# Kernel tuning notes

Measured on AMD Instinct MI355X. Metric: run time of the kernel, lower is better.

Reference implementation:

```python
import jax, jax.numpy as jnp
import numpy as np

B, S, HID = 2, 2048, 4096
NH, NKV, HD = 32, 8, 128
GRP = NH // NKV          # query heads per kv head
G = 128                  # weight quant group size
FP8_MAX = 448.0          # e4m3 max
EPS = 1e-6


def _rmsnorm(x, w):
    return x * jax.lax.rsqrt(jnp.mean(x * x, axis=-1, keepdims=True) + EPS) * w


def _act_quant(x):
    # per-token fp8 quantization: scale = amax/448, values clipped to fp8 range
    s = jnp.max(jnp.abs(x), axis=-1, keepdims=True) / FP8_MAX
    s = jnp.maximum(s, 1e-6)
    return jnp.clip(x / s, -FP8_MAX, FP8_MAX), s


def _deq_weight(wi4, wscale):
    # wi4: [out, in] int values in [0,16) -> signed int4 [-8,7]
    # wscale: [out, in//G] per-group scales, broadcast along input dim
    return (wi4.astype(jnp.float32) - 8.0) * jnp.repeat(wscale, G, axis=1)


def _rotate_half(x):
    x1, x2 = jnp.split(x, 2, axis=-1)
    return jnp.concatenate([-x2, x1], axis=-1)


def setup_inputs() -> dict:
    key = jax.random.key(0)
    ks = jax.random.split(key, 8)
    hidden_states = jax.random.normal(ks[0], (B, S, HID), dtype=jnp.float32)
    ln_weight = jnp.ones((HID,), dtype=jnp.float32)
    # real RoPE tables
    inv_freq = 1.0 / (10000.0 ** (np.arange(0, HD, 2, dtype=np.float32) / HD))
    ang = np.arange(S, dtype=np.float32)[:, None] * inv_freq[None, :]
    emb = np.concatenate([ang, ang], axis=-1)  # [S, HD]
    cos = jnp.broadcast_to(jnp.asarray(np.cos(emb)), (B, S, HD)).astype(jnp.float32)
    sin = jnp.broadcast_to(jnp.asarray(np.sin(emb)), (B, S, HD)).astype(jnp.float32)
    def wq(k, out, inp):
        ki, ksc = jax.random.split(k)
        wi = jax.random.randint(ki, (out, inp), 0, 16, dtype=jnp.int32)
        sc = jax.random.uniform(ksc, (out, inp // G), dtype=jnp.float32) * 0.01 + 0.001
        return wi, sc
    wq_i4, wq_scale = wq(ks[1], NH * HD, HID)
    wk_i4, wk_scale = wq(ks[2], NKV * HD, HID)
    wv_i4, wv_scale = wq(ks[3], NKV * HD, HID)
    wo_i4, wo_scale = wq(ks[4], HID, NH * HD)
    return dict(hidden_states=hidden_states, ln_weight=ln_weight, cos=cos, sin=sin,
                wq_scale=wq_scale, wk_scale=wk_scale, wv_scale=wv_scale, wo_scale=wo_scale,
                wq_i4=wq_i4, wk_i4=wk_i4, wv_i4=wv_i4, wo_i4=wo_i4)


def reference(hidden_states, ln_weight, cos, sin,
              wq_scale, wk_scale, wv_scale, wo_scale,
              wq_i4, wk_i4, wv_i4, wo_i4):
    b, s, _ = hidden_states.shape
    residual = hidden_states
    h = _rmsnorm(hidden_states, ln_weight)
    qx, qx_s = _act_quant(h)                     # [b,s,HID], [b,s,1]
    q = (qx @ _deq_weight(wq_i4, wq_scale).T) * qx_s
    k = (qx @ _deq_weight(wk_i4, wk_scale).T) * qx_s
    v = (qx @ _deq_weight(wv_i4, wv_scale).T) * qx_s
    q = q.reshape(b, s, NH, HD)
    k = k.reshape(b, s, NKV, HD)
    v = v.reshape(b, s, NKV, HD)
    cse, sne = cos[:, :, None, :], sin[:, :, None, :]
    q = q * cse + _rotate_half(q) * sne
    k = k * cse + _rotate_half(k) * sne
    # GQA causal attention (fp8 fmha numerics emulated in fp32)
    qg = q.reshape(b, s, NKV, GRP, HD)
    scaling = HD ** -0.5
    scores = jnp.einsum('bskgd,btkd->bkgst', qg, k) * scaling  # [b,kv,g,s,t]
    causal = jnp.tril(jnp.ones((s, s), dtype=bool))
    scores = jnp.where(causal, scores, jnp.float32(-1e30))
    p = jax.nn.softmax(scores, axis=-1)
    o = jnp.einsum('bkgst,btkd->bskgd', p, v).reshape(b, s, NH * HD)
    qo, qo_s = _act_quant(o)
    out = (qo @ _deq_weight(wo_i4, wo_scale).T) * qo_s + residual
    return out
```

## Files before the change

### kernel.cpp

```cpp
#include <hip/hip_runtime.h>
#include <stdint.h>

#define HID    4096
#define SLEN   2048
#define BATCH  2
#define NHEADS 32
#define NKVH   8
#define HDIM   128
#define NTOK   (BATCH*SLEN)
#define NQK    (NHEADS*HDIM)
#define NKVD   (NKVH*HDIM)
#define NQKV   (NQK + 2*NKVD)
#define ASTR   (NQK + NKVD)

typedef unsigned short u16;
typedef short short8 __attribute__((ext_vector_type(8)));
typedef float f32x4 __attribute__((ext_vector_type(4)));
typedef int int4v __attribute__((ext_vector_type(4)));
typedef u16 u16x4 __attribute__((ext_vector_type(4)));

static __device__ __forceinline__ u16 f2bf(float f) {
  unsigned u = __builtin_bit_cast(unsigned, f);
  u += 0x7FFFu + ((u >> 16) & 1u);
  return (u16)(u >> 16);
}
static __device__ __forceinline__ float bf2f(u16 h) {
  return __builtin_bit_cast(float, (unsigned)h << 16);
}
static __device__ __forceinline__ void gload_lds16(const void* g, void* l) {
  __builtin_amdgcn_global_load_lds((const __attribute__((address_space(1))) void*)g,
                                   (__attribute__((address_space(3))) void*)l, 16, 0, 0);
}

__global__ __launch_bounds__(256) void k_rmsnorm(const float* __restrict__ x,
                                                 const float* __restrict__ w,
                                                 u16* __restrict__ h) {
  const int row = blockIdx.x;
  const float4* xr = (const float4*)(x + (size_t)row * HID);
  float4 vals[4];
  float ss = 0.f;
#pragma unroll
  for (int i = 0; i < 4; ++i) {
    float4 v = xr[threadIdx.x + i * 256];
    vals[i] = v;
    ss += v.x*v.x + v.y*v.y + v.z*v.z + v.w*v.w;
  }
#pragma unroll
  for (int off = 32; off; off >>= 1) ss += __shfl_xor(ss, off);
  __shared__ float red[4];
  if ((threadIdx.x & 63) == 0) red[threadIdx.x >> 6] = ss;
  __syncthreads();
  ss = red[0] + red[1] + red[2] + red[3];
  const float scale = rsqrtf(ss * (1.f / HID) + 1e-6f);
  u16* hr = h + (size_t)row * HID;
#pragma unroll
  for (int i = 0; i < 4; ++i) {
    int c = (threadIdx.x + i * 256) * 4;
    float4 v = vals[i];
    unsigned lo = (unsigned)f2bf(v.x * scale * w[c])   | ((unsigned)f2bf(v.y * scale * w[c+1]) << 16);
    unsigned hi = (unsigned)f2bf(v.z * scale * w[c+2]) | ((unsigned)f2bf(v.w * scale * w[c+3]) << 16);
    *(unsigned long long*)(hr + c) = ((unsigned long long)hi << 32) | lo;
  }
}

__global__ __launch_bounds__(256) void k_deq(const int* __restrict__ W,
                                             const float* __restrict__ Ws,
                                             u16* __restrict__ out) {
  const int idx = blockIdx.x * 256 + threadIdx.x;
  const int n = idx >> 9;
  const int k8 = (idx & 511) * 8;
  const float sc = Ws[n * 32 + (k8 >> 7)];
  int4v a = *(const int4v*)(W + (size_t)n * HID + k8);
  int4v b = *(const int4v*)(W + (size_t)n * HID + k8 + 4);
  u16 r[8];
#pragma unroll
  for (int j = 0; j < 4; ++j) r[j]     = f2bf((float)(a[j] - 8) * sc);
#pragma unroll
  for (int j = 0; j < 4; ++j) r[j + 4] = f2bf((float)(b[j] - 8) * sc);
  *(short8*)(out + (size_t)n * HID + k8) = *(short8*)r;
}

#define BM 128
#define BN 128
#define BK 64

__global__ __launch_bounds__(256) void k_gemm_qkv_b(
    const u16* __restrict__ A, const u16* __restrict__ B,
    u16* __restrict__ C, u16* __restrict__ Vt) {
  __shared__ __align__(16) u16 lA[BM * BK];
  __shared__ __align__(16) u16 lB[BN * BK];
  const int tid = threadIdx.x;
  const int lane = tid & 63;
  const int wave = tid >> 6;
  const int wm = wave >> 1, wn = wave & 1;
  const int m0 = blockIdx.x * BM;
  const int n0 = blockIdx.y * BN;

  const int rloc = wave * 8 + (lane >> 3);
  const int lb8 = (((lane & 7) ^ (lane >> 3)) << 3);

  f32x4 acc[4][4];
#pragma unroll
  for (int mi = 0; mi < 4; ++mi)
#pragma unroll
    for (int ni = 0; ni < 4; ++ni) acc[mi][ni] = (f32x4){0.f, 0.f, 0.f, 0.f};

  for (int k0 = 0; k0 < HID; k0 += BK) {
    __syncthreads();
#pragma unroll
    for (int p = 0; p < 4; ++p)
      gload_lds16(A + (size_t)(m0 + p * 32 + rloc) * HID + k0 + lb8,
                  lA + p * 2048 + wave * 512);
#pragma unroll
    for (int p = 0; p < 4; ++p)
      gload_lds16(B + (size_t)(n0 + p * 32 + rloc) * HID + k0 + lb8,
                  lB + p * 2048 + wave * 512);
    __syncthreads();
#pragma unroll
    for (int kc = 0; kc < 2; ++kc) {
      const int kOff = kc * 32 + ((lane >> 4) << 3);
      short8 af[4], bfr[4];
#pragma unroll
      for (int i = 0; i < 4; ++i) {
        const int m = wm * 64 + i * 16 + (lane & 15);
        af[i] = *(const short8*)(lA + ((m * 64 + kOff) ^ ((m & 7) << 3)));
        const int n = wn * 64 + i * 16 + (lane & 15);
        bfr[i] = *(const short8*)(lB + ((n * 64 + kOff) ^ ((n & 7) << 3)));
      }
#pragma unroll
      for (int mi = 0; mi < 4; ++mi)
#pragma unroll
        for (int ni = 0; ni < 4; ++ni)
          acc[mi][ni] = __builtin_amdgcn_mfma_f32_16x16x32_bf16(af[mi], bfr[ni], acc[mi][ni], 0, 0, 0);
    }
  }
  if (n0 < ASTR) {
#pragma unroll
    for (int mi = 0; mi < 4; ++mi) {
      const int row = m0 + wm * 64 + mi * 16 + ((lane >> 4) << 2);
#pragma unroll
      for (int ni = 0; ni < 4; ++ni) {
        const int col = n0 + wn * 64 + ni * 16 + (lane & 15);
#pragma unroll
        for (int r = 0; r < 4; ++r)
          C[(size_t)(row + r) * ASTR + col] = f2bf(acc[mi][ni][r]);
      }
    }
  } else {
#pragma unroll
    for (int mi = 0; mi < 4; ++mi) {
      const int row = m0 + wm * 64 + mi * 16 + ((lane >> 4) << 2);
      const int b_ = row >> 11, s_ = row & 2047;
#pragma unroll
      for (int ni = 0; ni < 4; ++ni) {
        const int colv = (n0 - ASTR) + wn * 64 + ni * 16 + (lane & 15);
        u16x4 pk;
#pragma unroll
        for (int r = 0; r < 4; ++r) pk[r] = f2bf(acc[mi][ni][r]);
        *(u16x4*)(Vt + ((size_t)(b_ * NKVH + (colv >> 7)) * HDIM + (colv & 127)) * SLEN + s_) = pk;
      }
    }
  }
}

__global__ __launch_bounds__(256) void k_gemm_o_b(
    const u16* __restrict__ A, const u16* __restrict__ B,
    const float* __restrict__ resid, float* __restrict__ out) {
  __shared__ __align__(16) u16 lA[BM * BK];
  __shared__ __align__(16) u16 lB[BN * BK];
  const int tid = threadIdx.x;
  const int lane = tid & 63;
  const int wave = tid >> 6;
  const int wm = wave >> 1, wn = wave & 1;
  const int m0 = blockIdx.x * BM;
  const int n0 = blockIdx.y * BN;

  const int rloc = wave * 8 + (lane >> 3);
  const int lb8 = (((lane & 7) ^ (lane >> 3)) << 3);

  f32x4 acc[4][4];
#pragma unroll
  for (int mi = 0; mi < 4; ++mi)
#pragma unroll
    for (int ni = 0; ni < 4; ++ni) acc[mi][ni] = (f32x4){0.f, 0.f, 0.f, 0.f};

  for (int k0 = 0; k0 < NQK; k0 += BK) {
    __syncthreads();
#pragma unroll
    for (int p = 0; p < 4; ++p)
      gload_lds16(A + (size_t)(m0 + p * 32 + rloc) * NQK + k0 + lb8,
                  lA + p * 2048 + wave * 512);
#pragma unroll
    for (int p = 0; p < 4; ++p)
      gload_lds16(B + (size_t)(n0 + p * 32 + rloc) * NQK + k0 + lb8,
                  lB + p * 2048 + wave * 512);
    __syncthreads();
#pragma unroll
    for (int kc = 0; kc < 2; ++kc) {
      const int kOff = kc * 32 + ((lane >> 4) << 3);
      short8 af[4], bfr[4];
#pragma unroll
      for (int i = 0; i < 4; ++i) {
        const int m = wm * 64 + i * 16 + (lane & 15);
        af[i] = *(const short8*)(lA + ((m * 64 + kOff) ^ ((m & 7) << 3)));
        const int n = wn * 64 + i * 16 + (lane & 15);
        bfr[i] = *(const short8*)(lB + ((n * 64 + kOff) ^ ((n & 7) << 3)));
      }
#pragma unroll
      for (int mi = 0; mi < 4; ++mi)
#pragma unroll
        for (int ni = 0; ni < 4; ++ni)
          acc[mi][ni] = __builtin_amdgcn_mfma_f32_16x16x32_bf16(af[mi], bfr[ni], acc[mi][ni], 0, 0, 0);
    }
  }
#pragma unroll
  for (int mi = 0; mi < 4; ++mi) {
    const int row = m0 + wm * 64 + mi * 16 + ((lane >> 4) << 2);
#pragma unroll
    for (int ni = 0; ni < 4; ++ni) {
      const int col = n0 + wn * 64 + ni * 16 + (lane & 15);
#pragma unroll
      for (int r = 0; r < 4; ++r) {
        const size_t idx = (size_t)(row + r) * HID + col;
        out[idx] = acc[mi][ni][r] + resid[idx];
      }
    }
  }
}

__global__ __launch_bounds__(256) void k_gemm_qkv(
    const u16* __restrict__ A,
    const int* __restrict__ Wq, const int* __restrict__ Wk, const int* __restrict__ Wv,
    const float* __restrict__ Sq, const float* __restrict__ Sk, const float* __restrict__ Sv,
    u16* __restrict__ C, u16* __restrict__ Vt) {
  __shared__ __align__(16) u16 lA[BM * BK];
  __shared__ __align__(16) u16 lB[BN * BK];
  const int tid = threadIdx.x;
  const int lane = tid & 63;
  const int wave = tid >> 6;
  const int wm = wave >> 1, wn = wave & 1;
  const int m0 = blockIdx.x * BM;
  const int n0 = blockIdx.y * BN;

  const int* W; const float* Ws; int nb;
  if (n0 < NQK)       { W = Wq; Ws = Sq; nb = n0; }
  else if (n0 < ASTR) { W = Wk; Ws = Sk; nb = n0 - NQK; }
  else                { W = Wv; Ws = Sv; nb = n0 - ASTR; }

  const int mloc = wave * 8 + (lane >> 3);
  const int lb8 = (((lane & 7) ^ (lane >> 3)) << 3);

  f32x4 acc[4][4];
#pragma unroll
  for (int mi = 0; mi < 4; ++mi)
#pragma unroll
    for (int ni = 0; ni < 4; ++ni) acc[mi][ni] = (f32x4){0.f, 0.f, 0.f, 0.f};

  for (int k0 = 0; k0 < HID; k0 += BK) {
    __syncthreads();
#pragma unroll
    for (int p = 0; p < 4; ++p)
      gload_lds16(A + (size_t)(m0 + p * 32 + mloc) * HID + k0 + lb8,
                  lA + p * 2048 + wave * 512);
    const int grp = k0 >> 7;
#pragma unroll
    for (int p = 0; p < 8; ++p) {
      const int n = p * 16 + (tid >> 4);
      const int kk = (tid & 15) * 4;
      int4v wv4 = *(const int4v*)(W + (size_t)(nb + n) * HID + k0 + kk);
      const float sc = Ws[(nb + n) * 32 + grp];
      unsigned lo = (unsigned)f2bf((float)(wv4[0] - 8) * sc) |
                    ((unsigned)f2bf((float)(wv4[1] - 8) * sc) << 16);
      unsigned hi = (unsigned)f2bf((float)(wv4[2] - 8) * sc) |
                    ((unsigned)f2bf((float)(wv4[3] - 8) * sc) << 16);
      const int di = (n * 64 + kk) ^ ((n & 7) << 3);
      unsigned* dst = (unsigned*)(lB + di);
      dst[0] = lo; dst[1] = hi;
    }
    __syncthreads();
#pragma unroll
    for (int kc = 0; kc < 2; ++kc) {
      const int kOff = kc * 32 + ((lane >> 4) << 3);
      short8 af[4], bfr[4];
#pragma unroll
      for (int i = 0; i < 4; ++i) {
        const int m = wm * 64 + i * 16 + (lane & 15);
        af[i] = *(const short8*)(lA + ((m * 64 + kOff) ^ ((m & 7) << 3)));
        const int n = wn * 64 + i * 16 + (lane & 15);
        bfr[i] = *(const short8*)(lB + ((n * 64 + kOff) ^ ((n & 7) << 3)));
      }
#pragma unroll
      for (int mi = 0; mi < 4; ++mi)
#pragma unroll
        for (int ni = 0; ni < 4; ++ni)
          acc[mi][ni] = __builtin_amdgcn_mfma_f32_16x16x32_bf16(af[mi], bfr[ni], acc[mi][ni], 0, 0, 0);
    }
  }
  if (n0 < ASTR) {
#pragma unroll
    for (int mi = 0; mi < 4; ++mi) {
      const int row = m0 + wm * 64 + mi * 16 + ((lane >> 4) << 2);
#pragma unroll
      for (int ni = 0; ni < 4; ++ni) {
        const int col = n0 + wn * 64 + ni * 16 + (lane & 15);
#pragma unroll
        for (int r = 0; r < 4; ++r)
          C[(size_t)(row + r) * ASTR + col] = f2bf(acc[mi][ni][r]);
      }
    }
  } else {
#pragma unroll
    for (int mi = 0; mi < 4; ++mi) {
      const int row = m0 + wm * 64 + mi * 16 + ((lane >> 4) << 2);
      const int b_ = row >> 11, s_ = row & 2047;
#pragma unroll
      for (int ni = 0; ni < 4; ++ni) {
        const int colv = (n0 - ASTR) + wn * 64 + ni * 16 + (lane & 15);
        u16x4 pk;
#pragma unroll
        for (int r = 0; r < 4; ++r) pk[r] = f2bf(acc[mi][ni][r]);
        *(u16x4*)(Vt + ((size_t)(b_ * NKVH + (colv >> 7)) * HDIM + (colv & 127)) * SLEN + s_) = pk;
      }
    }
  }
}

__global__ __launch_bounds__(256) void k_gemm_o(
    const u16* __restrict__ A, const int* __restrict__ W, const float* __restrict__ Ws,
    const float* __restrict__ resid, float* __restrict__ out) {
  __shared__ __align__(16) u16 lA[BM * BK];
  __shared__ __align__(16) u16 lB[BN * BK];
  const int tid = threadIdx.x;
  const int lane = tid & 63;
  const int wave = tid >> 6;
  const int wm = wave >> 1, wn = wave & 1;
  const int m0 = blockIdx.x * BM;
  const int n0 = blockIdx.y * BN;

  const int mloc = wave * 8 + (lane >> 3);
  const int lb8 = (((lane & 7) ^ (lane >> 3)) << 3);

  f32x4 acc[4][4];
#pragma unroll
  for (int mi = 0; mi < 4; ++mi)
#pragma unroll
    for (int ni = 0; ni < 4; ++ni) acc[mi][ni] = (f32x4){0.f, 0.f, 0.f, 0.f};

  for (int k0 = 0; k0 < NQK; k0 += BK) {
    __syncthreads();
#pragma unroll
    for (int p = 0; p < 4; ++p)
      gload_lds16(A + (size_t)(m0 + p * 32 + mloc) * NQK + k0 + lb8,
                  lA + p * 2048 + wave * 512);
    const int grp = k0 >> 7;
#pragma unroll
    for (int p = 0; p < 8; ++p) {
      const int n = p * 16 + (tid >> 4);
      const int kk = (tid & 15) * 4;
      int4v wv4 = *(const int4v*)(W + (size_t)(n0 + n) * NQK + k0 + kk);
      const float sc = Ws[(n0 + n) * 32 + grp];
      unsigned lo = (unsigned)f2bf((float)(wv4[0] - 8) * sc) |
                    ((unsigned)f2bf((float)(wv4[1] - 8) * sc) << 16);
      unsigned hi = (unsigned)f2bf((float)(wv4[2] - 8) * sc) |
                    ((unsigned)f2bf((float)(wv4[3] - 8) * sc) << 16);
      const int di = (n * 64 + kk) ^ ((n & 7) << 3);
      unsigned* dst = (unsigned*)(lB + di);
      dst[0] = lo; dst[1] = hi;
    }
    __syncthreads();
#pragma unroll
    for (int kc = 0; kc < 2; ++kc) {
      const int kOff = kc * 32 + ((lane >> 4) << 3);
      short8 af[4], bfr[4];
#pragma unroll
      for (int i = 0; i < 4; ++i) {
        const int m = wm * 64 + i * 16 + (lane & 15);
        af[i] = *(const short8*)(lA + ((m * 64 + kOff) ^ ((m & 7) << 3)));
        const int n = wn * 64 + i * 16 + (lane & 15);
        bfr[i] = *(const short8*)(lB + ((n * 64 + kOff) ^ ((n & 7) << 3)));
      }
#pragma unroll
      for (int mi = 0; mi < 4; ++mi)
#pragma unroll
        for (int ni = 0; ni < 4; ++ni)
          acc[mi][ni] = __builtin_amdgcn_mfma_f32_16x16x32_bf16(af[mi], bfr[ni], acc[mi][ni], 0, 0, 0);
      }
  }
#pragma unroll
  for (int mi = 0; mi < 4; ++mi) {
    const int row = m0 + wm * 64 + mi * 16 + ((lane >> 4) << 2);
#pragma unroll
    for (int ni = 0; ni < 4; ++ni) {
      const int col = n0 + wn * 64 + ni * 16 + (lane & 15);
#pragma unroll
      for (int r = 0; r < 4; ++r) {
        const size_t idx = (size_t)(row + r) * HID + col;
        out[idx] = acc[mi][ni][r] + resid[idx];
      }
    }
  }
}

__global__ __launch_bounds__(256) void k_rope(u16* __restrict__ qk,
                                              const float* __restrict__ cosb,
                                              const float* __restrict__ sinb) {
  const int idx = blockIdx.x * 256 + threadIdx.x;
  const int d = idx & 63;
  const int hh = (idx >> 6) % 40;
  const int t = idx / (64 * 40);
  const int col = (hh < 32) ? hh * HDIM : NQK + (hh - 32) * HDIM;
  u16* p = qk + (size_t)t * ASTR + col;
  const float c = cosb[t * HDIM + d], s = sinb[t * HDIM + d];
  const float x1 = bf2f(p[d]), x2 = bf2f(p[d + 64]);
  p[d]      = f2bf(x1 * c - x2 * s);
  p[d + 64] = f2bf(x2 * c + x1 * s);
}

__global__ __launch_bounds__(256) void k_attn(const u16* __restrict__ qk,
                                              const u16* __restrict__ vt,
                                              u16* __restrict__ o) {
  const int slot = blockIdx.x;
  const int w = (slot & 7) * 128 + (slot >> 3);
  const int qi = 15 - (w & 15);
  const int h = (w >> 4) & 31;
  const int b = w >> 9;
  const int kvh = h >> 2;
  const int q0 = qi * 128;
  const int lane = threadIdx.x & 63, wave = threadIdx.x >> 6;
  const int m = lane & 15, kg = lane >> 4;

  const u16* Qb = qk + (size_t)b * SLEN * ASTR + h * HDIM;
  const u16* Kb = qk + (size_t)b * SLEN * ASTR + NQK + kvh * HDIM;
  const u16* Vb = vt + (size_t)(b * NKVH + kvh) * HDIM * SLEN;

  __shared__ __align__(16) u16 Kt[64 * 128];
  __shared__ __align__(16) u16 Vts[128 * 64];
  __shared__ __align__(16) u16 Pl[4][32 * 72];

  const int qr = q0 + wave * 32;
  short8 qf[2][4];
#pragma unroll
  for (int mi = 0; mi < 2; ++mi)
#pragma unroll
    for (int kc = 0; kc < 4; ++kc)
      qf[mi][kc] = *(const short8*)(Qb + (size_t)(qr + mi * 16 + m) * ASTR + kc * 32 + kg * 8);

  f32x4 oacc[2][8];
#pragma unroll
  for (int mi = 0; mi < 2; ++mi)
#pragma unroll
    for (int n = 0; n < 8; ++n) oacc[mi][n] = (f32x4){0.f, 0.f, 0.f, 0.f};
  float rm[2][4], rl[2][4];
#pragma unroll
  for (int mi = 0; mi < 2; ++mi)
#pragma unroll
    for (int r = 0; r < 4; ++r) { rm[mi][r] = -3.0e38f; rl[mi][r] = 0.f; }

  const float sscale = 0.08838834764831845f;
  const int nt = q0 / 64 + 2;
  for (int t = 0; t < nt; ++t) {
    const int kv0 = t * 64;
    __syncthreads();
#pragma unroll
    for (int p = 0; p < 4; ++p) {
      const int row = p * 16 + wave * 4 + (lane >> 4);
      const int c8s = (lane & 15) ^ (row & 7);
      gload_lds16(Kb + (size_t)(kv0 + row) * ASTR + c8s * 8, Kt + p * 2048 + wave * 512);
    }
#pragma unroll
    for (int p = 0; p < 4; ++p) {
      const int d = p * 32 + wave * 8 + (lane >> 3);
      const int c8s = (lane & 7) ^ (d & 7);
      gload_lds16(Vb + (size_t)d * SLEN + kv0 + c8s * 8, Vts + p * 2048 + wave * 512);
    }
    __syncthreads();

    f32x4 sf[2][4];
#pragma unroll
    for (int mi = 0; mi < 2; ++mi)
#pragma unroll
      for (int ni = 0; ni < 4; ++ni) sf[mi][ni] = (f32x4){0.f, 0.f, 0.f, 0.f};
#pragma unroll
    for (int ni = 0; ni < 4; ++ni)
#pragma unroll
      for (int kc = 0; kc < 4; ++kc) {
        const int krow = ni * 16 + m;
        short8 kf = *(const short8*)(Kt + krow * 128 + (((kc * 4 + kg) ^ (krow & 7)) << 3));
#pragma unroll
        for (int mi = 0; mi < 2; ++mi)
          sf[mi][ni] = __builtin_amdgcn_mfma_f32_16x16x32_bf16(qf[mi][kc], kf, sf[mi][ni], 0, 0, 0);
      }

#pragma unroll
    for (int mi = 0; mi < 2; ++mi) {
      const bool dg = (kv0 + 63 > qr + mi * 16);
      float tmax[4] = {-3.0e38f, -3.0e38f, -3.0e38f, -3.0e38f};
#pragma unroll
      for (int ni = 0; ni < 4; ++ni)
#pragma unroll
        for (int r = 0; r < 4; ++r) {
          float s = sf[mi][ni][r] * sscale;
          if (dg) {
            const int rowg = qr + mi * 16 + kg * 4 + r;
            const int colg = kv0 + ni * 16 + m;
            if (colg > rowg) s = -1e30f;
          }
          sf[mi][ni][r] = s;
          tmax[r] = fmaxf(tmax[r], s);
        }
#pragma unroll
      for (int r = 0; r < 4; ++r)
#pragma unroll
        for (int off = 1; off < 16; off <<= 1)
          tmax[r] = fmaxf(tmax[r], __shfl_xor(tmax[r], off));
      float scl[4], psum[4];
#pragma unroll
      for (int r = 0; r < 4; ++r) {
        const float mn = fmaxf(rm[mi][r], tmax[r]);
        scl[r] = __expf(rm[mi][r] - mn);
        rm[mi][r] = mn;
        psum[r] = 0.f;
      }
#pragma unroll
      for (int ni = 0; ni < 4; ++ni)
#pragma unroll
        for (int r = 0; r < 4; ++r) {
          const float p = __expf(sf[mi][ni][r] - rm[mi][r]);
          psum[r] += p;
          Pl[wave][(mi * 16 + kg * 4 + r) * 72 + ni * 16 + m] = f2bf(p);
        }
#pragma unroll
      for (int r = 0; r < 4; ++r) {
#pragma unroll
        for (int off = 1; off < 16; off <<= 1)
          psum[r] += __shfl_xor(psum[r], off);
        rl[mi][r] = rl[mi][r] * scl[r] + psum[r];
      }
#pragma unroll
      for (int n = 0; n < 8; ++n)
#pragma unroll
        for (int r = 0; r < 4; ++r) oacc[mi][n][r] *= scl[r];
    }

#pragma unroll
    for (int kc = 0; kc < 2; ++kc) {
      short8 pf[2];
#pragma unroll
      for (int mi = 0; mi < 2; ++mi)
        pf[mi] = *(const short8*)(&Pl[wave][(mi * 16 + m) * 72 + kc * 32 + kg * 8]);
#pragma unroll
      for (int n = 0; n < 8; ++n) {
        const int vrow = n * 16 + m;
        short8 vf = *(const short8*)(Vts + vrow * 64 + (((kc * 4 + kg) ^ (vrow & 7)) << 3));
#pragma unroll
        for (int mi = 0; mi < 2; ++mi)
          oacc[mi][n] = __builtin_amdgcn_mfma_f32_16x16x32_bf16(pf[mi], vf, oacc[mi][n], 0, 0, 0);
      }
    }
  }

#pragma unroll
  for (int mi = 0; mi < 2; ++mi) {
    float inv[4];
#pragma unroll
    for (int r = 0; r < 4; ++r) inv[r] = 1.0f / rl[mi][r];
#pragma unroll
    for (int n = 0; n < 8; ++n)
#pragma unroll
      for (int r = 0; r < 4; ++r) {
        const int row = qr + mi * 16 + kg * 4 + r;
        o[((size_t)b * SLEN + row) * NQK + h * HDIM + n * 16 + m] = f2bf(oacc[mi][n][r] * inv[r]);
      }
  }
}

extern "C" void kernel_launch(void* const* d_in, const int* in_sizes, int n_in,
                              void* d_out, int out_size, void* d_ws, size_t ws_size,
                              hipStream_t stream) {
  (void)in_sizes; (void)n_in; (void)out_size;
  const float* x    = (const float*)d_in[0];
  const float* lnw  = (const float*)d_in[1];
  const float* cosb = (const float*)d_in[2];
  const float* sinb = (const float*)d_in[3];
  const float* sq   = (const float*)d_in[4];
  const float* sk   = (const float*)d_in[5];
  const float* sv   = (const float*)d_in[6];
  const float* so   = (const float*)d_in[7];
  const int* wq     = (const int*)d_in[8];
  const int* wk     = (const int*)d_in[9];
  const int* wv     = (const int*)d_in[10];
  const int* wo     = (const int*)d_in[11];

  u16* h   = (u16*)d_ws;
  u16* qkb = h + (size_t)NTOK * HID;
  u16* vtb = qkb + (size_t)NTOK * ASTR;
  u16* wqkvb = vtb + (size_t)BATCH * NKVH * HDIM * SLEN;
  u16* wob   = wqkvb + (size_t)NQKV * HID;
  float* out = (float*)d_out;

  const size_t need = ((size_t)NTOK * HID + (size_t)NTOK * ASTR +
                       (size_t)BATCH * NKVH * HDIM * SLEN +
                       (size_t)NQKV * HID + (size_t)HID * NQK) * sizeof(u16);
  const bool predeq = (ws_size >= need);

  k_rmsnorm<<<NTOK, 256, 0, stream>>>(x, lnw, h);

  if (predeq) {
    k_deq<<<NQK  * 2, 256, 0, stream>>>(wq, sq, wqkvb);
    k_deq<<<NKVD * 2, 256, 0, stream>>>(wk, sk, wqkvb + (size_t)NQK * HID);
    k_deq<<<NKVD * 2, 256, 0, stream>>>(wv, sv, wqkvb + (size_t)ASTR * HID);
    k_deq<<<NQK  * 2, 256, 0, stream>>>(wo, so, wob);
    dim3 g1(NTOK / BM, NQKV / BN);
    k_gemm_qkv_b<<<g1, 256, 0, stream>>>(h, wqkvb, qkb, vtb);
  } else {
    dim3 g1(NTOK / BM, NQKV / BN);
    k_gemm_qkv<<<g1, 256, 0, stream>>>(h, wq, wk, wv, sq, sk, sv, qkb, vtb);
  }

  k_rope<<<(NTOK * 40 * 64) / 256, 256, 0, stream>>>(qkb, cosb, sinb);

  k_attn<<<1024, 256, 0, stream>>>(qkb, vtb, h);

  dim3 g3(NTOK / BM, HID / BN);
  if (predeq) {
    k_gemm_o_b<<<g3, 256, 0, stream>>>(h, wob, x, out);
  } else {
    k_gemm_o<<<g3, 256, 0, stream>>>(h, wo, so, x, out);
  }
}
```

Baseline: 765.8 us.

## Fuse weight dequant launches, fold softmax scale into RoPE, lazy rescale attention

The four weight-dequant launches become one kernel that picks the source tensor by row. The softmax scale times log2(e) is folded into the Q RoPE output, so attention can use exp2f with no per-score multiply. Attention now reads K fragments straight from global memory instead of staging them in LDS, and it skips the online-softmax rescale unless the running max grows by more than a threshold. Reading K from global may add memory latency and redundant loads across waves, and the lazy rescale changes numerics slightly. The removed barrier before the score compute also relies on the later barrier for V visibility.

```diff
diff --git a/kernel.cpp b/kernel.cpp
--- a/kernel.cpp
+++ b/kernel.cpp
@@ -63,21 +63,29 @@
   }
 }
 
-__global__ __launch_bounds__(256) void k_deq(const int* __restrict__ W,
-                                             const float* __restrict__ Ws,
-                                             u16* __restrict__ out) {
+__global__ __launch_bounds__(256) void k_deq_all(
+    const int* __restrict__ wq, const int* __restrict__ wk,
+    const int* __restrict__ wv, const int* __restrict__ wo,
+    const float* __restrict__ sq, const float* __restrict__ sk,
+    const float* __restrict__ sv, const float* __restrict__ so,
+    u16* __restrict__ out) {
   const int idx = blockIdx.x * 256 + threadIdx.x;
-  const int n = idx >> 9;
+  const int row = idx >> 9;
   const int k8 = (idx & 511) * 8;
-  const float sc = Ws[n * 32 + (k8 >> 7)];
-  int4v a = *(const int4v*)(W + (size_t)n * HID + k8);
-  int4v b = *(const int4v*)(W + (size_t)n * HID + k8 + 4);
-  u16 r[8];
-#pragma unroll
-  for (int j = 0; j < 4; ++j) r[j]     = f2bf((float)(a[j] - 8) * sc);
-#pragma unroll
-  for (int j = 0; j < 4; ++j) r[j + 4] = f2bf((float)(b[j] - 8) * sc);
-  *(short8*)(out + (size_t)n * HID + k8) = *(short8*)r;
+  const int* W; const float* S; int r;
+  if (row < 4096)      { W = wq; S = sq; r = row; }
+  else if (row < 5120) { W = wk; S = sk; r = row - 4096; }
+  else if (row < 6144) { W = wv; S = sv; r = row - 5120; }
+  else                 { W = wo; S = so; r = row - 6144; }
+  const float sc = S[r * 32 + (k8 >> 7)];
+  int4v a = *(const int4v*)(W + (size_t)r * HID + k8);
+  int4v b = *(const int4v*)(W + (size_t)r * HID + k8 + 4);
+  u16 rr[8];
+#pragma unroll
+  for (int j = 0; j < 4; ++j) rr[j]     = f2bf((float)(a[j] - 8) * sc);
+#pragma unroll
+  for (int j = 0; j < 4; ++j) rr[j + 4] = f2bf((float)(b[j] - 8) * sc);
+  *(short8*)(out + (size_t)row * HID + k8) = *(short8*)rr;
 }
 
 #define BM 128
@@ -409,11 +417,12 @@
   const int hh = (idx >> 6) % 40;
   const int t = idx / (64 * 40);
   const int col = (hh < 32) ? hh * HDIM : NQK + (hh - 32) * HDIM;
+  const float qs = (hh < 32) ? 0.12751744f : 1.0f;
   u16* p = qk + (size_t)t * ASTR + col;
   const float c = cosb[t * HDIM + d], s = sinb[t * HDIM + d];
   const float x1 = bf2f(p[d]), x2 = bf2f(p[d + 64]);
-  p[d]      = f2bf(x1 * c - x2 * s);
-  p[d + 64] = f2bf(x2 * c + x1 * s);
+  p[d]      = f2bf((x1 * c - x2 * s) * qs);
+  p[d + 64] = f2bf((x2 * c + x1 * s) * qs);
 }
 
 __global__ __launch_bounds__(256) void k_attn(const u16* __restrict__ qk,
@@ -433,7 +442,6 @@
   const u16* Kb = qk + (size_t)b * SLEN * ASTR + NQK + kvh * HDIM;
   const u16* Vb = vt + (size_t)(b * NKVH + kvh) * HDIM * SLEN;
 
-  __shared__ __align__(16) u16 Kt[64 * 128];
   __shared__ __align__(16) u16 Vts[128 * 64];
   __shared__ __align__(16) u16 Pl[4][32 * 72];
 
@@ -456,24 +464,17 @@
 #pragma unroll
     for (int r = 0; r < 4; ++r) { rm[mi][r] = -3.0e38f; rl[mi][r] = 0.f; }
 
-  const float sscale = 0.08838834764831845f;
   const int nt = q0 / 64 + 2;
   for (int t = 0; t < nt; ++t) {
     const int kv0 = t * 64;
     __syncthreads();
-#pragma unroll
-    for (int p = 0; p < 4; ++p) {
-      const int row = p * 16 + wave * 4 + (lane >> 4);
-      const int c8s = (lane & 15) ^ (row & 7);
-      gload_lds16(Kb + (size_t)(kv0 + row) * ASTR + c8s * 8, Kt + p * 2048 + wave * 512);
-    }
+
 #pragma unroll
     for (int p = 0; p < 4; ++p) {
       const int d = p * 32 + wave * 8 + (lane >> 3);
       const int c8s = (lane & 7) ^ (d & 7);
       gload_lds16(Vb + (size_t)d * SLEN + kv0 + c8s * 8, Vts + p * 2048 + wave * 512);
     }
-    __syncthreads();
 
     f32x4 sf[2][4];
 #pragma unroll
@@ -481,15 +482,16 @@
 #pragma unroll
       for (int ni = 0; ni < 4; ++ni) sf[mi][ni] = (f32x4){0.f, 0.f, 0.f, 0.f};
 #pragma unroll
-    for (int ni = 0; ni < 4; ++ni)
+    for (int ni = 0; ni < 4; ++ni) {
+      const u16* kr = Kb + (size_t)(kv0 + ni * 16 + m) * ASTR + kg * 8;
 #pragma unroll
       for (int kc = 0; kc < 4; ++kc) {
-        const int krow = ni * 16 + m;
-        short8 kf = *(const short8*)(Kt + krow * 128 + (((kc * 4 + kg) ^ (krow & 7)) << 3));
+        short8 kf = *(const short8*)(kr + kc * 32);
 #pragma unroll
         for (int mi = 0; mi < 2; ++mi)
           sf[mi][ni] = __builtin_amdgcn_mfma_f32_16x16x32_bf16(qf[mi][kc], kf, sf[mi][ni], 0, 0, 0);
       }
+    }
 
 #pragma unroll
     for (int mi = 0; mi < 2; ++mi) {
@@ -499,7 +501,7 @@
       for (int ni = 0; ni < 4; ++ni)
 #pragma unroll
         for (int r = 0; r < 4; ++r) {
-          float s = sf[mi][ni][r] * sscale;
+          float s = sf[mi][ni][r];
           if (dg) {
             const int rowg = qr + mi * 16 + kg * 4 + r;
             const int colg = kv0 + ni * 16 + m;
@@ -513,19 +515,31 @@
 #pragma unroll
         for (int off = 1; off < 16; off <<= 1)
           tmax[r] = fmaxf(tmax[r], __shfl_xor(tmax[r], off));
-      float scl[4], psum[4];
-#pragma unroll
-      for (int r = 0; r < 4; ++r) {
-        const float mn = fmaxf(rm[mi][r], tmax[r]);
-        scl[r] = __expf(rm[mi][r] - mn);
-        rm[mi][r] = mn;
-        psum[r] = 0.f;
-      }
+
+      bool need = false;
+#pragma unroll
+      for (int r = 0; r < 4; ++r) need |= (tmax[r] > rm[mi][r] + 11.5f);
+      if (__any(need)) {
+        float scl[4];
+#pragma unroll
+        for (int r = 0; r < 4; ++r) {
+          const float mn = fmaxf(rm[mi][r], tmax[r]);
+          scl[r] = exp2f(rm[mi][r] - mn);
+          rm[mi][r] = mn;
+          rl[mi][r] *= scl[r];
+        }
+#pragma unroll
+        for (int n = 0; n < 8; ++n)
+#pragma unroll
+          for (int r = 0; r < 4; ++r) oacc[mi][n][r] *= scl[r];
+      }
+
+      float psum[4] = {0.f, 0.f, 0.f, 0.f};
 #pragma unroll
       for (int ni = 0; ni < 4; ++ni)
 #pragma unroll
         for (int r = 0; r < 4; ++r) {
-          const float p = __expf(sf[mi][ni][r] - rm[mi][r]);
+          const float p = exp2f(sf[mi][ni][r] - rm[mi][r]);
           psum[r] += p;
           Pl[wave][(mi * 16 + kg * 4 + r) * 72 + ni * 16 + m] = f2bf(p);
         }
@@ -534,13 +548,11 @@
 #pragma unroll
         for (int off = 1; off < 16; off <<= 1)
           psum[r] += __shfl_xor(psum[r], off);
-        rl[mi][r] = rl[mi][r] * scl[r] + psum[r];
-      }
-#pragma unroll
-      for (int n = 0; n < 8; ++n)
-#pragma unroll
-        for (int r = 0; r < 4; ++r) oacc[mi][n][r] *= scl[r];
-    }
+        rl[mi][r] += psum[r];
+      }
+    }
+
+    __syncthreads();
 
 #pragma unroll
     for (int kc = 0; kc < 2; ++kc) {
@@ -606,10 +618,7 @@
   k_rmsnorm<<<NTOK, 256, 0, stream>>>(x, lnw, h);
 
   if (predeq) {
-    k_deq<<<NQK  * 2, 256, 0, stream>>>(wq, sq, wqkvb);
-    k_deq<<<NKVD * 2, 256, 0, stream>>>(wk, sk, wqkvb + (size_t)NQK * HID);
-    k_deq<<<NKVD * 2, 256, 0, stream>>>(wv, sv, wqkvb + (size_t)ASTR * HID);
-    k_deq<<<NQK  * 2, 256, 0, stream>>>(wo, so, wob);
+    k_deq_all<<<(10240 * 512) / 256, 256, 0, stream>>>(wq, wk, wv, wo, sq, sk, sv, so, wqkvb);
     dim3 g1(NTOK / BM, NQKV / BN);
     k_gemm_qkv_b<<<g1, 256, 0, stream>>>(h, wqkvb, qkb, vtb);
   } else {
@@ -621,10 +630,11 @@
 
   k_attn<<<1024, 256, 0, stream>>>(qkb, vtb, h);
 
-  dim3 g3(NTOK / BM, HID / BN);
   if (predeq) {
+    dim3 g3(NTOK / BM, HID / BN);
     k_gemm_o_b<<<g3, 256, 0, stream>>>(h, wob, x, out);
   } else {
+    dim3 g3(NTOK / BM, HID / BN);
     k_gemm_o<<<g3, 256, 0, stream>>>(h, wo, so, x, out);
   }
 }
```

Result: slower. 956.4 us (+24.9%).
